# Performance work log

Measured on AMD Instinct MI355X. Metric: run time of the kernel, lower is better.

## Reference

```python
import jax, jax.numpy as jnp
import numpy as np

N = 10000      # nodes
D_IN = 12      # exact in-degree per node (regular graph -> static triplet count)
E = N * D_IN   # 120000 directed edges
T = E * D_IN   # 1440000 triplets (k->i for each edge i->j)
K_R = 16
K_A = 8
HID = 64
OUT = 32
R_GAMMA = 8.0  # 1/(2*((4.0-0.0)/16)**2)
A_GAMMA = 8.0  # 1/(2*(2.0/8)**2)
EPS = 1e-8


def setup_inputs() -> dict:
    rng = np.random.default_rng(0)
    # edge e: row[e] -> col[e]; edges sorted by destination so in-edges of node i are [i*D_IN,(i+1)*D_IN)
    col = np.repeat(np.arange(N, dtype=np.int64), D_IN)
    row = rng.integers(0, N, size=E, dtype=np.int64)
    # triplets: for each edge e (i=row[e], j=col[e]), all D_IN edges k->i
    e_e = np.repeat(np.arange(E, dtype=np.int64), D_IN)                      # [T]
    ki_idx = (row[:, None] * D_IN + np.arange(D_IN)[None, :]).reshape(-1)    # [T] indices of k->i edges
    k_e = row[ki_idx]
    i_e = row[e_e]
    j_e = col[e_e]

    key = jax.random.key(0)
    kp, k1, k2 = jax.random.split(key, 3)
    pos = jax.random.normal(kp, (N, 3), dtype=jnp.float32) * 2.0
    in_dim = 2 * K_R + K_A
    W1 = jax.random.normal(k1, (in_dim, HID), dtype=jnp.float32) / np.sqrt(in_dim)
    b1 = jnp.zeros((HID,), dtype=jnp.float32)
    W2 = jax.random.normal(k2, (HID, OUT), dtype=jnp.float32) / np.sqrt(HID)
    b2 = jnp.zeros((OUT,), dtype=jnp.float32)
    r_centers = jnp.linspace(0.0, 4.0, K_R, dtype=jnp.float32)
    a_centers = jnp.linspace(-1.0, 1.0, K_A, dtype=jnp.float32)
    return {
        "pos": pos, "W1": W1, "b1": b1, "W2": W2, "b2": b2,
        "r_centers": r_centers, "a_centers": a_centers,
        "e_e": jnp.asarray(e_e, dtype=jnp.int32),
        "i_e": jnp.asarray(i_e, dtype=jnp.int32),
        "j_e": jnp.asarray(j_e, dtype=jnp.int32),
        "k_e": jnp.asarray(k_e, dtype=jnp.int32),
    }


def _rbf(x, centers, gamma):
    # x: [T,1], centers: [K] -> [T,K]
    return jnp.exp(-gamma * (x - centers[None, :]) ** 2)


def reference(pos, W1, b1, W2, b2, r_centers, a_centers, e_e, i_e, j_e, k_e):
    rij = pos[j_e] - pos[i_e]                 # [T,3]
    rik = pos[k_e] - pos[i_e]                 # [T,3]
    dij = jnp.linalg.norm(rij, axis=-1, keepdims=True)
    dik = jnp.linalg.norm(rik, axis=-1, keepdims=True)
    cos_theta = jnp.clip(jnp.sum(rij * rik, axis=-1, keepdims=True) / (dij * dik + EPS), -1.0, 1.0)
    feat = jnp.concatenate(
        [_rbf(dij, r_centers, R_GAMMA), _rbf(dik, r_centers, R_GAMMA), _rbf(cos_theta, a_centers, A_GAMMA)],
        axis=-1,
    )                                          # [T, 2*K_R+K_A]
    h = jax.nn.silu(feat @ W1 + b1)            # [T, HID]
    emb = h @ W2 + b2                          # [T, OUT]
    # exclude k == j triplets (torch masks them out before scatter)
    emb = emb * (k_e != j_e)[:, None].astype(emb.dtype)
    return jax.ops.segment_sum(emb, e_e, num_segments=E)  # [E, OUT]
```

## Files before the change

### kernel.cpp

```cpp
#include <hip/hip_runtime.h>
#include <hip/hip_bf16.h>
#include <math.h>

#define N_GROUPS 7500
#define HID 64
#define OUTC 32
#define EPSV 1e-8f
#define C2G  (-11.54156032f)
#define LOG2E 1.44269504f
#define CSR  (4.0f / 15.0f)
#define CSA  (2.0f / 7.0f)

typedef __bf16 bf16x8 __attribute__((ext_vector_type(8)));
typedef float  f32x4  __attribute__((ext_vector_type(4)));
typedef unsigned short u16x4 __attribute__((ext_vector_type(4)));

#define WAVES 4
#define BLOCK 256
#define GRID 1875

__global__ __launch_bounds__(BLOCK, 4) void gemnet_mfma_kernel(
    const float* __restrict__ pos,
    const float* __restrict__ W1, const float* __restrict__ b1,
    const float* __restrict__ W2, const float* __restrict__ b2,
    const int* __restrict__ i_e, const int* __restrict__ k_e,
    float* __restrict__ out)
{
    __shared__ __align__(16) unsigned short hbuf[WAVES][2][16 * HID];

    const int tid  = threadIdx.x;
    const int w    = tid >> 6;
    const int lane = tid & 63;
    const int tl16 = lane & 15;
    const int g    = lane >> 4;
    const int sw   = (tl16 & 7) << 3;

    bf16x8 a1[4][2];
#pragma unroll
    for (int mt = 0; mt < 4; ++mt) {
#pragma unroll
        for (int e = 0; e < 8; ++e) {
            a1[mt][0][e] = (__bf16)W1[(g * 8 + e) * HID + mt * 16 + tl16];
            float v1 = 0.0f;
            if (e < 2) v1 = W1[(32 + 2 * g + e) * HID + mt * 16 + tl16];
            if (e == 7 && g == 0) v1 = b1[mt * 16 + tl16];
            a1[mt][1][e] = (__bf16)v1;
        }
    }
    bf16x8 a2[2][2];
#pragma unroll
    for (int mt = 0; mt < 2; ++mt)
#pragma unroll
        for (int ks = 0; ks < 2; ++ks)
#pragma unroll
            for (int e = 0; e < 8; ++e)
                a2[mt][ks][e] = (__bf16)W2[(ks * 32 + g * 8 + e) * OUTC + mt * 16 + tl16];

    bf16x8 bf1t;
#pragma unroll
    for (int e = 0; e < 8; ++e)
        bf1t[e] = (__bf16)((e == 7 && g == 0) ? 1.0f : 0.0f);

    const f32x4 fz = {0.f, 0.f, 0.f, 0.f};
    const float gofs_r = (float)(8 * (g & 1)) * CSR;
    const float gofs_a = (float)(2 * g) * CSA - 1.0f;

    const int grp    = blockIdx.x * WAVES + w;
    const int e_lane = grp * 16 + tl16;
    const int tlane  = e_lane * 12;
    const int j      = e_lane / 12;

    const int   i   = i_e[tlane];
    const float pix = pos[3 * i], piy = pos[3 * i + 1], piz = pos[3 * i + 2];
    const float rijx = pos[3 * j] - pix, rijy = pos[3 * j + 1] - piy, rijz = pos[3 * j + 2] - piz;
    const float dij = __builtin_amdgcn_sqrtf(rijx * rijx + rijy * rijy + rijz * rijz);

    f32x4 D0, D1;
#pragma unroll
    for (int r = 0; r < 4; ++r) { D0[r] = b2[4 * g + r]; D1[r] = b2[16 + 4 * g + r]; }

#pragma unroll
    for (int m = 0; m < 12; ++m) {
        const int k = k_e[tlane + m];

        const float rikx = pos[3 * k] - pix, riky = pos[3 * k + 1] - piy, rikz = pos[3 * k + 2] - piz;
        const float dik = __builtin_amdgcn_sqrtf(rikx * rikx + riky * riky + rikz * rikz);
        const float dotv = rijx * rikx + rijy * riky + rijz * rikz;
        float cosv = dotv * __builtin_amdgcn_rcpf(dij * dik + EPSV);
        cosv = fminf(1.0f, fmaxf(-1.0f, cosv));

        const float dco = ((g < 2) ? dij : dik) - gofs_r;
        const float Aq  = C2G * dco * dco;
        const float Bn  = (-2.0f * C2G * CSR) * dco;
        bf16x8 bf0;
#pragma unroll
        for (int e = 0; e < 8; ++e) {
            const float arg = fmaf((float)e, Bn, Aq) + (C2G * CSR * CSR) * (float)(e * e);
            bf0[e] = (__bf16)__builtin_amdgcn_exp2f(arg);
        }
        bf16x8 bf1 = bf1t;
        const float cco = cosv - gofs_a;
        bf1[0] = (__bf16)__builtin_amdgcn_exp2f(C2G * cco * cco);
        const float cc1 = cco - CSA;
        bf1[1] = (__bf16)__builtin_amdgcn_exp2f(C2G * cc1 * cc1);

        f32x4 acc1[4];
#pragma unroll
        for (int mt = 0; mt < 4; ++mt) {
            acc1[mt] = __builtin_amdgcn_mfma_f32_16x16x32_bf16(a1[mt][0], bf0, fz, 0, 0, 0);
            acc1[mt] = __builtin_amdgcn_mfma_f32_16x16x32_bf16(a1[mt][1], bf1, acc1[mt], 0, 0, 0);
        }

        const u16x4 hz = {0, 0, 0, 0};
        const bool keep = (k != j);
#pragma unroll
        for (int mt = 0; mt < 4; ++mt) {
            u16x4 hw;
#pragma unroll
            for (int r = 0; r < 4; ++r) {
                const float v = acc1[mt][r];
                const float sv = v * __builtin_amdgcn_rcpf(1.0f + __builtin_amdgcn_exp2f(-LOG2E * v));
                hw[r] = __builtin_bit_cast(unsigned short, (__bf16)sv);
            }
            hw = keep ? hw : hz;
            const int colW = (mt * 16 + 4 * g) ^ sw;
            *(u16x4*)&hbuf[w][m & 1][tl16 * HID + colW] = hw;
        }
        const bf16x8 hb0 = *(const bf16x8*)&hbuf[w][m & 1][tl16 * HID + ((8 * g) ^ sw)];
        const bf16x8 hb1 = *(const bf16x8*)&hbuf[w][m & 1][tl16 * HID + ((32 + 8 * g) ^ sw)];

        D0 = __builtin_amdgcn_mfma_f32_16x16x32_bf16(a2[0][0], hb0, D0, 0, 0, 0);
        D0 = __builtin_amdgcn_mfma_f32_16x16x32_bf16(a2[0][1], hb1, D0, 0, 0, 0);
        D1 = __builtin_amdgcn_mfma_f32_16x16x32_bf16(a2[1][0], hb0, D1, 0, 0, 0);
        D1 = __builtin_amdgcn_mfma_f32_16x16x32_bf16(a2[1][1], hb1, D1, 0, 0, 0);
    }

    const int rbase = e_lane * OUTC;
    *(f32x4*)&out[rbase + 4 * g]      = D0;
    *(f32x4*)&out[rbase + 16 + 4 * g] = D1;
}

extern "C" void kernel_launch(void* const* d_in, const int* in_sizes, int n_in,
                              void* d_out, int out_size, void* d_ws, size_t ws_size,
                              hipStream_t stream) {
    const float* pos = (const float*)d_in[0];
    const float* W1  = (const float*)d_in[1];
    const float* b1  = (const float*)d_in[2];
    const float* W2  = (const float*)d_in[3];
    const float* b2  = (const float*)d_in[4];
    const int* i_e = (const int*)d_in[8];
    const int* k_e = (const int*)d_in[10];
    float* out = (float*)d_out;

    gemnet_mfma_kernel<<<GRID, BLOCK, 0, stream>>>(
        pos, W1, b1, W2, b2, i_e, k_e, out);
}
```

Baseline: 50.45 us.

## Hoist loop-invariant dij RBF contribution out of triplet loop, halve first-layer MFMAs

The first-layer GEMM is split into an edge-invariant part (the dij RBF features plus bias), computed once per edge via MFMA before the loop, and a per-triplet part (the dik RBF and the angle features) packed into a single K=32 MFMA that accumulates onto the hoisted result. This halves the first-layer MFMAs and the per-triplet exp2 count. The k indices are also loaded as three int4 vectors up front instead of one scalar load per iteration. It adds register pressure from the accu and kv arrays and needs 16-byte alignment of k_e at tlane, which holds because tlane is a multiple of 12.

New measurement: 46.00 us. 1.1x faster.

```diff
diff --git a/kernel.cpp b/kernel.cpp
--- a/kernel.cpp
+++ b/kernel.cpp
@@ -35,16 +35,27 @@
     const int g    = lane >> 4;
     const int sw   = (tl16 & 7) << 3;
 
-    bf16x8 a1[4][2];
+    bf16x8 a1d[4];
 #pragma unroll
     for (int mt = 0; mt < 4; ++mt) {
 #pragma unroll
         for (int e = 0; e < 8; ++e) {
-            a1[mt][0][e] = (__bf16)W1[(g * 8 + e) * HID + mt * 16 + tl16];
-            float v1 = 0.0f;
-            if (e < 2) v1 = W1[(32 + 2 * g + e) * HID + mt * 16 + tl16];
-            if (e == 7 && g == 0) v1 = b1[mt * 16 + tl16];
-            a1[mt][1][e] = (__bf16)v1;
+            float v = 0.0f;
+            if (e < 4)       v = W1[(16 + 4 * g + e) * HID + mt * 16 + tl16];
+            else if (e == 4) v = W1[(32 + 2 * g) * HID + mt * 16 + tl16];
+            else if (e == 5) v = W1[(32 + 2 * g + 1) * HID + mt * 16 + tl16];
+            a1d[mt][e] = (__bf16)v;
+        }
+    }
+    bf16x8 au[4];
+#pragma unroll
+    for (int mt = 0; mt < 4; ++mt) {
+#pragma unroll
+        for (int e = 0; e < 8; ++e) {
+            float v = 0.0f;
+            if (e < 4)                 v = W1[(4 * g + e) * HID + mt * 16 + tl16];
+            else if (e == 4 && g == 0) v = b1[mt * 16 + tl16];
+            au[mt][e] = (__bf16)v;
         }
     }
     bf16x8 a2[2][2];
@@ -56,24 +67,44 @@
             for (int e = 0; e < 8; ++e)
                 a2[mt][ks][e] = (__bf16)W2[(ks * 32 + g * 8 + e) * OUTC + mt * 16 + tl16];
 
-    bf16x8 bf1t;
-#pragma unroll
-    for (int e = 0; e < 8; ++e)
-        bf1t[e] = (__bf16)((e == 7 && g == 0) ? 1.0f : 0.0f);
-
     const f32x4 fz = {0.f, 0.f, 0.f, 0.f};
-    const float gofs_r = (float)(8 * (g & 1)) * CSR;
-    const float gofs_a = (float)(2 * g) * CSA - 1.0f;
+    const float gofs_r4 = (float)(4 * g) * CSR;
+    const float gofs_a  = (float)(2 * g) * CSA - 1.0f;
 
     const int grp    = blockIdx.x * WAVES + w;
     const int e_lane = grp * 16 + tl16;
     const int tlane  = e_lane * 12;
     const int j      = e_lane / 12;
 
+    const int4 kq0 = *(const int4*)&k_e[tlane];
+    const int4 kq1 = *(const int4*)&k_e[tlane + 4];
+    const int4 kq2 = *(const int4*)&k_e[tlane + 8];
+    const int kv[12] = {kq0.x, kq0.y, kq0.z, kq0.w,
+                        kq1.x, kq1.y, kq1.z, kq1.w,
+                        kq2.x, kq2.y, kq2.z, kq2.w};
+
     const int   i   = i_e[tlane];
     const float pix = pos[3 * i], piy = pos[3 * i + 1], piz = pos[3 * i + 2];
     const float rijx = pos[3 * j] - pix, rijy = pos[3 * j + 1] - piy, rijz = pos[3 * j + 2] - piz;
     const float dij = __builtin_amdgcn_sqrtf(rijx * rijx + rijy * rijy + rijz * rijz);
+
+    bf16x8 bu;
+    {
+        const float dco = dij - gofs_r4;
+#pragma unroll
+        for (int e = 0; e < 8; ++e) {
+            float v = 0.0f;
+            if (e < 4) {
+                const float x = dco - (float)e * CSR;
+                v = __builtin_amdgcn_exp2f(C2G * x * x);
+            } else if (e == 4 && g == 0) v = 1.0f;
+            bu[e] = (__bf16)v;
+        }
+    }
+    f32x4 accu[4];
+#pragma unroll
+    for (int mt = 0; mt < 4; ++mt)
+        accu[mt] = __builtin_amdgcn_mfma_f32_16x16x32_bf16(au[mt], bu, fz, 0, 0, 0);
 
     f32x4 D0, D1;
 #pragma unroll
@@ -81,7 +112,7 @@
 
 #pragma unroll
     for (int m = 0; m < 12; ++m) {
-        const int k = k_e[tlane + m];
+        const int k = kv[m];
 
         const float rikx = pos[3 * k] - pix, riky = pos[3 * k + 1] - piy, rikz = pos[3 * k + 2] - piz;
         const float dik = __builtin_amdgcn_sqrtf(rikx * rikx + riky * riky + rikz * rikz);
@@ -89,27 +120,26 @@
         float cosv = dotv * __builtin_amdgcn_rcpf(dij * dik + EPSV);
         cosv = fminf(1.0f, fmaxf(-1.0f, cosv));
 
-        const float dco = ((g < 2) ? dij : dik) - gofs_r;
+        const float dco = dik - gofs_r4;
         const float Aq  = C2G * dco * dco;
         const float Bn  = (-2.0f * C2G * CSR) * dco;
-        bf16x8 bf0;
+        bf16x8 bm;
 #pragma unroll
-        for (int e = 0; e < 8; ++e) {
+        for (int e = 0; e < 4; ++e) {
             const float arg = fmaf((float)e, Bn, Aq) + (C2G * CSR * CSR) * (float)(e * e);
-            bf0[e] = (__bf16)__builtin_amdgcn_exp2f(arg);
+            bm[e] = (__bf16)__builtin_amdgcn_exp2f(arg);
         }
-        bf16x8 bf1 = bf1t;
         const float cco = cosv - gofs_a;
-        bf1[0] = (__bf16)__builtin_amdgcn_exp2f(C2G * cco * cco);
+        bm[4] = (__bf16)__builtin_amdgcn_exp2f(C2G * cco * cco);
         const float cc1 = cco - CSA;
-        bf1[1] = (__bf16)__builtin_amdgcn_exp2f(C2G * cc1 * cc1);
+        bm[5] = (__bf16)__builtin_amdgcn_exp2f(C2G * cc1 * cc1);
+        bm[6] = (__bf16)0.0f;
+        bm[7] = (__bf16)0.0f;
 
         f32x4 acc1[4];
 #pragma unroll
-        for (int mt = 0; mt < 4; ++mt) {
-            acc1[mt] = __builtin_amdgcn_mfma_f32_16x16x32_bf16(a1[mt][0], bf0, fz, 0, 0, 0);
-            acc1[mt] = __builtin_amdgcn_mfma_f32_16x16x32_bf16(a1[mt][1], bf1, acc1[mt], 0, 0, 0);
-        }
+        for (int mt = 0; mt < 4; ++mt)
+            acc1[mt] = __builtin_amdgcn_mfma_f32_16x16x32_bf16(a1d[mt], bm, accu[mt], 0, 0, 0);
 
         const u16x4 hz = {0, 0, 0, 0};
         const bool keep = (k != j);
```
